# Performance work log

Hardware: AMD Instinct MI355X
Metric: run time of the kernel (lower is better)

Reference implementation:

```python
import jax, jax.numpy as jnp
import numpy as np

N_NODES = 100000
N_EDGES = 3200000
N_GRAPHS = 1024
IN_DIM, HID, OUT = 1, 32, 32
BN_EPS = 1e-5


def setup_inputs() -> dict:
    key = jax.random.key(0)
    ks = jax.random.split(key, 12)
    inp = {
        "x": jax.random.normal(ks[0], (N_NODES, IN_DIM), dtype=jnp.float32),
        "edge_index": jax.random.randint(ks[1], (2, N_EDGES), 0, N_NODES, dtype=jnp.int64),
        "batch": jnp.sort(jax.random.randint(ks[2], (N_NODES,), 0, N_GRAPHS, dtype=jnp.int64)),
        # GCNConv linear weights (out = x @ W + b) and BatchNorm (eval-mode) params
        "W1": jax.random.normal(ks[3], (IN_DIM, HID), dtype=jnp.float32) / np.sqrt(IN_DIM),
        "b1": jnp.zeros((HID,), jnp.float32),
        "bn1_g": jnp.ones((HID,), jnp.float32),
        "bn1_b": jnp.zeros((HID,), jnp.float32),
        "bn1_m": jax.random.normal(ks[4], (HID,), dtype=jnp.float32) * 0.1,
        "bn1_v": jnp.ones((HID,), jnp.float32),
        "W2": jax.random.normal(ks[5], (HID, HID), dtype=jnp.float32) / np.sqrt(HID),
        "b2": jnp.zeros((HID,), jnp.float32),
        "bn2_g": jnp.ones((HID,), jnp.float32),
        "bn2_b": jnp.zeros((HID,), jnp.float32),
        "bn2_m": jax.random.normal(ks[6], (HID,), dtype=jnp.float32) * 0.1,
        "bn2_v": jnp.ones((HID,), jnp.float32),
        "W3": jax.random.normal(ks[7], (HID, OUT), dtype=jnp.float32) / np.sqrt(HID),
        "b3": jnp.zeros((OUT,), jnp.float32),
    }
    return inp


def _gcn_norm(edge_index, n_nodes):
    # add self loops, compute sym-normalized edge weights (PyG GCNConv default)
    loop = jnp.arange(n_nodes, dtype=edge_index.dtype)
    src = jnp.concatenate([edge_index[0], loop])
    dst = jnp.concatenate([edge_index[1], loop])
    deg = jax.ops.segment_sum(jnp.ones_like(dst, dtype=jnp.float32), dst, num_segments=n_nodes)
    dinv = jnp.where(deg > 0, jax.lax.rsqrt(deg), 0.0)
    norm = dinv[src] * dinv[dst]  # [E + N]
    return src, dst, norm


def _gcn_conv(x, src, dst, norm, W, b, n_nodes):
    h = x @ W                                   # [N, F_out]
    msg = h[src] * norm[:, None]                # gather + scale, [E+N, F_out]
    out = jax.ops.segment_sum(msg, dst, num_segments=n_nodes)  # scatter-add
    return out + b


def _bn_eval(x, g, b, m, v):
    return (x - m) * jax.lax.rsqrt(v + BN_EPS) * g + b


def reference(x, edge_index, batch, W1, b1, bn1_g, bn1_b, bn1_m, bn1_v,
              W2, b2, bn2_g, bn2_b, bn2_m, bn2_v, W3, b3):
    n = x.shape[0]
    src, dst, norm = _gcn_norm(edge_index, n)
    h = _gcn_conv(x, src, dst, norm, W1, b1, n)
    h = jax.nn.relu(_bn_eval(h, bn1_g, bn1_b, bn1_m, bn1_v))  # dropout = id (eval)
    h = _gcn_conv(h, src, dst, norm, W2, b2, n)
    h = jax.nn.relu(_bn_eval(h, bn2_g, bn2_b, bn2_m, bn2_v))
    h = _gcn_conv(h, src, dst, norm, W3, b3, n)
    # global mean pool over graphs
    sums = jax.ops.segment_sum(h, batch, num_segments=N_GRAPHS)
    cnts = jax.ops.segment_sum(jnp.ones((n,), h.dtype), batch, num_segments=N_GRAPHS)
    return sums / jnp.maximum(cnts, 1.0)[:, None]
```

## Files before the change

kernel.cpp:

```cpp
#include <hip/hip_runtime.h>

#define N_NODES 100000
#define N_EDGES 3200000
#define N_GRAPHS 1024
#define HID 32
#define BN_EPS 1e-5f
#define NB 256

#define NBKT 512
#define NPB 196
#define PART_TILE 4096
#define PART_THREADS 256
#define PART_EPT (PART_TILE / PART_THREADS)


__device__ __forceinline__ int lbound(const int* __restrict__ a, int n, int key) {
    int lo = 0, hi = n;
    while (lo < hi) {
        int mid = (lo + hi) >> 1;
        if (a[mid] < key) lo = mid + 1; else hi = mid;
    }
    return lo;
}

__device__ __forceinline__ float bf2f(unsigned short h) {
    return __uint_as_float((unsigned)h << 16);
}
__device__ __forceinline__ unsigned short f2bf(float x) {
    unsigned u = __float_as_uint(x);
    u += 0x7fffu + ((u >> 16) & 1u);
    return (unsigned short)(u >> 16);
}


__global__ void k_zero(int* __restrict__ bhist) {
    bhist[threadIdx.x] = 0;
}

__global__ void k_hist(const int* __restrict__ dst, int* __restrict__ bhist) {
    __shared__ int h[NBKT];
    for (int i = threadIdx.x; i < NBKT; i += NB) h[i] = 0;
    __syncthreads();
    for (int e = blockIdx.x * NB + threadIdx.x; e < N_EDGES; e += gridDim.x * NB)
        atomicAdd(&h[dst[e] / NPB], 1);
    __syncthreads();
    for (int i = threadIdx.x; i < NBKT; i += NB)
        if (h[i]) atomicAdd(&bhist[i], h[i]);
}

__global__ void k_scan512(const int* __restrict__ bhist, int* __restrict__ bstart,
                          int* __restrict__ bcursor) {
    __shared__ int sm[NBKT];
    int t = threadIdx.x;
    int orig = bhist[t];
    sm[t] = orig;
    __syncthreads();
    for (int off = 1; off < NBKT; off <<= 1) {
        int v = (t >= off) ? sm[t - off] : 0;
        __syncthreads();
        sm[t] += v;
        __syncthreads();
    }
    int ex = sm[t] - orig;
    bstart[t] = ex;
    bcursor[t] = ex;
    if (t == NBKT - 1) bstart[NBKT] = sm[t];
}

__global__ void k_partition(const int* __restrict__ src, const int* __restrict__ dst,
                            int* __restrict__ bcursor,
                            unsigned long long* __restrict__ ebuf) {
    __shared__ int lh[NBKT];
    __shared__ int lcur[NBKT];
    const int tile0 = blockIdx.x * PART_TILE;
    for (int i = threadIdx.x; i < NBKT; i += PART_THREADS) lh[i] = 0;
    __syncthreads();
    int s[PART_EPT], d[PART_EPT], bk[PART_EPT];
#pragma unroll
    for (int k = 0; k < PART_EPT; ++k) {
        int e = tile0 + k * PART_THREADS + threadIdx.x;
        bool ok = (e < N_EDGES);
        s[k] = ok ? src[e] : 0;
        d[k] = ok ? dst[e] : 0;
        bk[k] = ok ? (d[k] / NPB) : -1;
        if (ok) atomicAdd(&lh[bk[k]], 1);
    }
    __syncthreads();
    for (int i = threadIdx.x; i < NBKT; i += PART_THREADS)
        lcur[i] = lh[i] ? atomicAdd(&bcursor[i], lh[i]) : 0;
    __syncthreads();
#pragma unroll
    for (int k = 0; k < PART_EPT; ++k) {
        if (bk[k] >= 0) {
            int pos = atomicAdd(&lcur[bk[k]], 1);
            ebuf[pos] = ((unsigned long long)(unsigned)d[k] << 32) | (unsigned)s[k];
        }
    }
}

__global__ void k_bucket(const int* __restrict__ bstart,
                         const unsigned long long* __restrict__ ebuf,
                         const float* __restrict__ x,
                         int* __restrict__ rowstart, int* __restrict__ deg,
                         float* __restrict__ dinv, float* __restrict__ zs1,
                         int* __restrict__ csr) {
    __shared__ int hist[NPB];
    __shared__ int sm[256];
    __shared__ int lcur[NPB];
    const int b = blockIdx.x;
    const int node0 = b * NPB;
    const int nn = N_NODES - node0;
    const int elo = bstart[b], ehi = bstart[b + 1];
    const int t = threadIdx.x;

    for (int i = t; i < NPB; i += blockDim.x) hist[i] = 0;
    __syncthreads();
    for (int e = elo + t; e < ehi; e += blockDim.x) {
        int dv = (int)(ebuf[e] >> 32);
        atomicAdd(&hist[dv - node0], 1);
    }
    __syncthreads();
    int orig = 0;
    if (t < 256) { orig = (t < NPB) ? hist[t] : 0; sm[t] = orig; }
    __syncthreads();
    for (int off = 1; off < 256; off <<= 1) {
        int v = 0;
        if (t < 256 && t >= off) v = sm[t - off];
        __syncthreads();
        if (t < 256) sm[t] += v;
        __syncthreads();
    }
    if (t < NPB) {
        int ex = sm[t] - orig;
        lcur[t] = ex;
        if (t < nn) {
            int node = node0 + t;
            rowstart[node] = elo + ex;
            deg[node] = orig;
            float di = rsqrtf((float)(orig + 1));
            dinv[node] = di;
            zs1[node] = di * x[node];
        }
    }
    __syncthreads();
    for (int e = elo + t; e < ehi; e += blockDim.x) {
        unsigned long long pk = ebuf[e];
        int dv = (int)(pk >> 32) - node0;
        int pos = atomicAdd(&lcur[dv], 1);
        csr[elo + pos] = (int)(pk & 0xffffffffu);
    }
}


__global__ void k_gather1(const int* __restrict__ rowstart, const int* __restrict__ deg,
                          const int* __restrict__ csr, const float* __restrict__ dinv,
                          const float* __restrict__ zs1, float* __restrict__ s) {
    int v = blockIdx.x * NB + threadIdx.x;
    if (v < N_NODES) {
        int lo = rowstart[v], n = deg[v];
        float acc = zs1[v];
        int j = 0;
        for (; j + 4 <= n; j += 4) {
            int u0 = csr[lo + j], u1 = csr[lo + j + 1];
            int u2 = csr[lo + j + 2], u3 = csr[lo + j + 3];
            float a0 = zs1[u0], a1 = zs1[u1], a2 = zs1[u2], a3 = zs1[u3];
            acc += (a0 + a1) + (a2 + a3);
        }
        for (; j < n; ++j) acc += zs1[csr[lo + j]];
        s[v] = dinv[v] * acc;
    }
}

__global__ void k_l1post(const float* __restrict__ s, const float* __restrict__ W1,
                         const float* __restrict__ b1, const float* __restrict__ g,
                         const float* __restrict__ bb, const float* __restrict__ m,
                         const float* __restrict__ v, const float* __restrict__ dinv,
                         unsigned short* __restrict__ zs2h) {
    int t = blockIdx.x * NB + threadIdx.x;
    if (t < N_NODES * HID) {
        int i = t >> 5, f = t & 31;
        float h = s[i] * W1[f] + b1[f];
        float scale = g[f] * rsqrtf(v[f] + BN_EPS);
        float z = fmaxf((h - m[f]) * scale + bb[f], 0.0f);
        zs2h[t] = f2bf(dinv[i] * z);
    }
}


__global__ void k_gather2(const int* __restrict__ rowstart, const int* __restrict__ deg,
                          const int* __restrict__ csr, const float* __restrict__ dinv,
                          const unsigned short* __restrict__ zs2h,
                          const float* __restrict__ W2,
                          const float* __restrict__ b2, const float* __restrict__ g2,
                          const float* __restrict__ bb2, const float* __restrict__ m2,
                          const float* __restrict__ v2, unsigned short* __restrict__ zs3h) {
    __shared__ float Ws[HID * HID];
    __shared__ float rowbuf[NB / HID][HID + 1];
    for (int k = threadIdx.x; k < HID * HID; k += NB) Ws[k] = W2[k];

    int t = blockIdx.x * NB + threadIdx.x;
    int v = t >> 5, f = t & 31, r = threadIdx.x >> 5;
    float acc = 0.0f, di = 0.0f;
    if (v < N_NODES) {
        di = dinv[v];
        int lo = rowstart[v], n = deg[v];
        acc = bf2f(zs2h[v * HID + f]);
        int j = 0;
        for (; j + 4 <= n; j += 4) {
            int u0 = csr[lo + j], u1 = csr[lo + j + 1];
            int u2 = csr[lo + j + 2], u3 = csr[lo + j + 3];
            float a0 = bf2f(zs2h[u0 * HID + f]);
            float a1 = bf2f(zs2h[u1 * HID + f]);
            float a2 = bf2f(zs2h[u2 * HID + f]);
            float a3 = bf2f(zs2h[u3 * HID + f]);
            acc += (a0 + a1) + (a2 + a3);
        }
        for (; j < n; ++j) acc += bf2f(zs2h[csr[lo + j] * HID + f]);
        acc *= di;
    }
    rowbuf[r][f] = acc;
    __syncthreads();
    if (v < N_NODES) {
        float h = b2[f];
#pragma unroll
        for (int k = 0; k < HID; ++k) h += rowbuf[r][k] * Ws[k * HID + f];
        float scale = g2[f] * rsqrtf(v2[f] + BN_EPS);
        float z = fmaxf((h - m2[f]) * scale + bb2[f], 0.0f);
        zs3h[v * HID + f] = f2bf(di * z);
    }
}


__global__ void k_gather3(const int* __restrict__ rowstart, const int* __restrict__ deg,
                          const int* __restrict__ csr, const float* __restrict__ dinv,
                          const unsigned short* __restrict__ zs3h,
                          float* __restrict__ agg3) {
    int t = blockIdx.x * NB + threadIdx.x;
    int v = t >> 5, f = t & 31;
    if (v < N_NODES) {
        int lo = rowstart[v], n = deg[v];
        float acc = bf2f(zs3h[v * HID + f]);
        int j = 0;
        for (; j + 4 <= n; j += 4) {
            int u0 = csr[lo + j], u1 = csr[lo + j + 1];
            int u2 = csr[lo + j + 2], u3 = csr[lo + j + 3];
            float a0 = bf2f(zs3h[u0 * HID + f]);
            float a1 = bf2f(zs3h[u1 * HID + f]);
            float a2 = bf2f(zs3h[u2 * HID + f]);
            float a3 = bf2f(zs3h[u3 * HID + f]);
            acc += (a0 + a1) + (a2 + a3);
        }
        for (; j < n; ++j) acc += bf2f(zs3h[csr[lo + j] * HID + f]);
        agg3[v * HID + f] = dinv[v] * acc;
    }
}


__global__ void k_pool(const float* __restrict__ agg3, const int* __restrict__ batch,
                       const float* __restrict__ W3, const float* __restrict__ b3,
                       float* __restrict__ out) {
    __shared__ float Ws[HID * HID];
    __shared__ float part[NB / HID][HID + 1];
    __shared__ float mrow[HID];
    int g = blockIdx.x;
    for (int k = threadIdx.x; k < HID * HID; k += NB) Ws[k] = W3[k];

    int lo = lbound(batch, N_NODES, g);
    int hi = lbound(batch, N_NODES, g + 1);

    int r = threadIdx.x >> 5, f = threadIdx.x & 31;
    float acc = 0.0f;
    for (int i = lo + r; i < hi; i += NB / HID) acc += agg3[i * HID + f];
    part[r][f] = acc;
    __syncthreads();
    if (threadIdx.x < HID) {
        float srow = 0.0f;
#pragma unroll
        for (int k = 0; k < NB / HID; ++k) srow += part[k][threadIdx.x];
        float c = (float)(hi - lo);
        mrow[threadIdx.x] = (hi > lo) ? srow / c : 0.0f;
    }
    __syncthreads();
    if (threadIdx.x < HID) {
        int ff = threadIdx.x;
        float o = 0.0f;
        if (hi > lo) {
            o = b3[ff];
#pragma unroll
            for (int k = 0; k < HID; ++k) o += mrow[k] * Ws[k * HID + ff];
        }
        out[g * HID + ff] = o;
    }
}


extern "C" void kernel_launch(void* const* d_in, const int* in_sizes, int n_in,
                              void* d_out, int out_size, void* d_ws, size_t ws_size,
                              hipStream_t stream) {
    const float* x     = (const float*)d_in[0];
    const int*   eidx  = (const int*)d_in[1];
    const int*   batch = (const int*)d_in[2];
    const float* W1    = (const float*)d_in[3];
    const float* b1    = (const float*)d_in[4];
    const float* bn1g  = (const float*)d_in[5];
    const float* bn1b  = (const float*)d_in[6];
    const float* bn1m  = (const float*)d_in[7];
    const float* bn1v  = (const float*)d_in[8];
    const float* W2    = (const float*)d_in[9];
    const float* b2    = (const float*)d_in[10];
    const float* bn2g  = (const float*)d_in[11];
    const float* bn2b  = (const float*)d_in[12];
    const float* bn2m  = (const float*)d_in[13];
    const float* bn2v  = (const float*)d_in[14];
    const float* W3    = (const float*)d_in[15];
    const float* b3    = (const float*)d_in[16];
    float* out = (float*)d_out;

    const int* src = eidx;
    const int* dst = eidx + N_EDGES;

    char* ws = (char*)d_ws;
    size_t off = 0;
    auto carve = [&](size_t bytes) {
        void* p = ws + off;
        off += (bytes + 255) & ~size_t(255);
        return p;
    };
    int*   bhist    = (int*)carve(NBKT * 4);
    int*   bstart   = (int*)carve((NBKT + 1) * 4);
    int*   bcursor  = (int*)carve(NBKT * 4);
    int*   rowstart = (int*)carve(N_NODES * 4);
    int*   deg      = (int*)carve(N_NODES * 4);
    float* dinv     = (float*)carve(N_NODES * 4);
    float* zs1      = (float*)carve(N_NODES * 4);
    float* s        = (float*)carve(N_NODES * 4);
    int*   csr      = (int*)carve((size_t)N_EDGES * 4);
    char*  region   = (char*)carve((size_t)N_EDGES * 8);
    unsigned long long* ebuf = (unsigned long long*)region;
    unsigned short* zs2h = (unsigned short*)region;
    unsigned short* zs3h = (unsigned short*)(region + (size_t)N_NODES * HID * 2);
    float* agg3          = (float*)(region + (size_t)N_NODES * HID * 4);

    const int gN   = (N_NODES + NB - 1) / NB;
    const int gNF  = (N_NODES * HID + NB - 1) / NB;
    const int gPart = (N_EDGES + PART_TILE - 1) / PART_TILE;

    k_zero<<<1, NBKT, 0, stream>>>(bhist);
    k_hist<<<1024, NB, 0, stream>>>(dst, bhist);
    k_scan512<<<1, NBKT, 0, stream>>>(bhist, bstart, bcursor);
    k_partition<<<gPart, PART_THREADS, 0, stream>>>(src, dst, bcursor, ebuf);
    k_bucket<<<NBKT, 512, 0, stream>>>(bstart, ebuf, x, rowstart, deg, dinv, zs1, csr);
    k_gather1<<<gN, NB, 0, stream>>>(rowstart, deg, csr, dinv, zs1, s);
    k_l1post<<<gNF, NB, 0, stream>>>(s, W1, b1, bn1g, bn1b, bn1m, bn1v, dinv, zs2h);
    k_gather2<<<gNF, NB, 0, stream>>>(rowstart, deg, csr, dinv, zs2h,
                                      W2, b2, bn2g, bn2b, bn2m, bn2v, zs3h);
    k_gather3<<<gNF, NB, 0, stream>>>(rowstart, deg, csr, dinv, zs3h, agg3);
    k_pool<<<N_GRAPHS, NB, 0, stream>>>(agg3, batch, W3, b3, out);
}
```

Before: 282.4 us.

## Fuse layer-1 post into gather2, pack edges to 32-bit, bf16 agg3, nontemporal loads

Removes the k_l1post kernel. gather2 now recomputes each neighbour's layer-1 activation on the fly from a packed (s*dinv, dinv) float2, so it never materialises or reads the bf16 N×32 zs2 buffer. The partition buffer shrinks from 64-bit to 32-bit entries (local dst offset in the high bits, src in the low 17 bits). The layer-3 aggregate is stored as bf16, the gather loops unroll to 8, and streaming index reads use nontemporal loads. These cut memory traffic and one launch, at the cost of extra per-edge ALU work in gather2 and lower precision in the pooled aggregate.

```diff
diff --git a/kernel.cpp b/kernel.cpp
--- a/kernel.cpp
+++ b/kernel.cpp
@@ -42,7 +42,7 @@
     for (int i = threadIdx.x; i < NBKT; i += NB) h[i] = 0;
     __syncthreads();
     for (int e = blockIdx.x * NB + threadIdx.x; e < N_EDGES; e += gridDim.x * NB)
-        atomicAdd(&h[dst[e] / NPB], 1);
+        atomicAdd(&h[__builtin_nontemporal_load(&dst[e]) / NPB], 1);
     __syncthreads();
     for (int i = threadIdx.x; i < NBKT; i += NB)
         if (h[i]) atomicAdd(&bhist[i], h[i]);
@@ -68,21 +68,22 @@
 }
 
 __global__ void k_partition(const int* __restrict__ src, const int* __restrict__ dst,
-                            int* __restrict__ bcursor,
-                            unsigned long long* __restrict__ ebuf) {
+                            int* __restrict__ bcursor, unsigned* __restrict__ ebuf) {
     __shared__ int lh[NBKT];
     __shared__ int lcur[NBKT];
     const int tile0 = blockIdx.x * PART_TILE;
     for (int i = threadIdx.x; i < NBKT; i += PART_THREADS) lh[i] = 0;
     __syncthreads();
-    int s[PART_EPT], d[PART_EPT], bk[PART_EPT];
+    int s[PART_EPT], bk[PART_EPT], dl[PART_EPT];
 #pragma unroll
     for (int k = 0; k < PART_EPT; ++k) {
         int e = tile0 + k * PART_THREADS + threadIdx.x;
         bool ok = (e < N_EDGES);
-        s[k] = ok ? src[e] : 0;
-        d[k] = ok ? dst[e] : 0;
-        bk[k] = ok ? (d[k] / NPB) : -1;
+        int sv = ok ? __builtin_nontemporal_load(&src[e]) : 0;
+        int dv = ok ? __builtin_nontemporal_load(&dst[e]) : 0;
+        s[k] = sv;
+        bk[k] = ok ? (dv / NPB) : -1;
+        dl[k] = dv - bk[k] * NPB;
         if (ok) atomicAdd(&lh[bk[k]], 1);
     }
     __syncthreads();
@@ -93,13 +94,13 @@
     for (int k = 0; k < PART_EPT; ++k) {
         if (bk[k] >= 0) {
             int pos = atomicAdd(&lcur[bk[k]], 1);
-            ebuf[pos] = ((unsigned long long)(unsigned)d[k] << 32) | (unsigned)s[k];
+            ebuf[pos] = ((unsigned)dl[k] << 17) | (unsigned)s[k];
         }
     }
 }
 
 __global__ void k_bucket(const int* __restrict__ bstart,
-                         const unsigned long long* __restrict__ ebuf,
+                         const unsigned* __restrict__ ebuf,
                          const float* __restrict__ x,
                          int* __restrict__ rowstart, int* __restrict__ deg,
                          float* __restrict__ dinv, float* __restrict__ zs1,
@@ -115,10 +116,8 @@
 
     for (int i = t; i < NPB; i += blockDim.x) hist[i] = 0;
     __syncthreads();
-    for (int e = elo + t; e < ehi; e += blockDim.x) {
-        int dv = (int)(ebuf[e] >> 32);
-        atomicAdd(&hist[dv - node0], 1);
-    }
+    for (int e = elo + t; e < ehi; e += blockDim.x)
+        atomicAdd(&hist[ebuf[e] >> 17], 1);
     __syncthreads();
     int orig = 0;
     if (t < 256) { orig = (t < NPB) ? hist[t] : 0; sm[t] = orig; }
@@ -144,52 +143,40 @@
     }
     __syncthreads();
     for (int e = elo + t; e < ehi; e += blockDim.x) {
-        unsigned long long pk = ebuf[e];
-        int dv = (int)(pk >> 32) - node0;
-        int pos = atomicAdd(&lcur[dv], 1);
-        csr[elo + pos] = (int)(pk & 0xffffffffu);
+        unsigned pk = ebuf[e];
+        int pos = atomicAdd(&lcur[pk >> 17], 1);
+        csr[elo + pos] = (int)(pk & 0x1FFFFu);
     }
 }
 
 
 __global__ void k_gather1(const int* __restrict__ rowstart, const int* __restrict__ deg,
                           const int* __restrict__ csr, const float* __restrict__ dinv,
-                          const float* __restrict__ zs1, float* __restrict__ s) {
+                          const float* __restrict__ zs1, float2* __restrict__ sd) {
     int v = blockIdx.x * NB + threadIdx.x;
     if (v < N_NODES) {
         int lo = rowstart[v], n = deg[v];
         float acc = zs1[v];
         int j = 0;
         for (; j + 4 <= n; j += 4) {
-            int u0 = csr[lo + j], u1 = csr[lo + j + 1];
-            int u2 = csr[lo + j + 2], u3 = csr[lo + j + 3];
+            int u0 = __builtin_nontemporal_load(&csr[lo + j]);
+            int u1 = __builtin_nontemporal_load(&csr[lo + j + 1]);
+            int u2 = __builtin_nontemporal_load(&csr[lo + j + 2]);
+            int u3 = __builtin_nontemporal_load(&csr[lo + j + 3]);
             float a0 = zs1[u0], a1 = zs1[u1], a2 = zs1[u2], a3 = zs1[u3];
             acc += (a0 + a1) + (a2 + a3);
         }
         for (; j < n; ++j) acc += zs1[csr[lo + j]];
-        s[v] = dinv[v] * acc;
-    }
-}
-
-__global__ void k_l1post(const float* __restrict__ s, const float* __restrict__ W1,
-                         const float* __restrict__ b1, const float* __restrict__ g,
-                         const float* __restrict__ bb, const float* __restrict__ m,
-                         const float* __restrict__ v, const float* __restrict__ dinv,
-                         unsigned short* __restrict__ zs2h) {
-    int t = blockIdx.x * NB + threadIdx.x;
-    if (t < N_NODES * HID) {
-        int i = t >> 5, f = t & 31;
-        float h = s[i] * W1[f] + b1[f];
-        float scale = g[f] * rsqrtf(v[f] + BN_EPS);
-        float z = fmaxf((h - m[f]) * scale + bb[f], 0.0f);
-        zs2h[t] = f2bf(dinv[i] * z);
-    }
-}
-
+        float di = dinv[v];
+        sd[v] = make_float2(di * acc, di);
+    }
+}
 
 __global__ void k_gather2(const int* __restrict__ rowstart, const int* __restrict__ deg,
-                          const int* __restrict__ csr, const float* __restrict__ dinv,
-                          const unsigned short* __restrict__ zs2h,
+                          const int* __restrict__ csr, const float2* __restrict__ sd,
+                          const float* __restrict__ W1, const float* __restrict__ b1,
+                          const float* __restrict__ g1, const float* __restrict__ bb1,
+                          const float* __restrict__ m1, const float* __restrict__ v1,
                           const float* __restrict__ W2,
                           const float* __restrict__ b2, const float* __restrict__ g2,
                           const float* __restrict__ bb2, const float* __restrict__ m2,
@@ -200,22 +187,41 @@
 
     int t = blockIdx.x * NB + threadIdx.x;
     int v = t >> 5, f = t & 31, r = threadIdx.x >> 5;
+    float sc1 = g1[f] * rsqrtf(v1[f] + BN_EPS);
+    float A = W1[f] * sc1;
+    float Bc = (b1[f] - m1[f]) * sc1 + bb1[f];
     float acc = 0.0f, di = 0.0f;
     if (v < N_NODES) {
-        di = dinv[v];
+        float2 pv = sd[v];
+        di = pv.y;
+        acc = di * fmaxf(pv.x * A + Bc, 0.0f);
         int lo = rowstart[v], n = deg[v];
-        acc = bf2f(zs2h[v * HID + f]);
         int j = 0;
-        for (; j + 4 <= n; j += 4) {
-            int u0 = csr[lo + j], u1 = csr[lo + j + 1];
-            int u2 = csr[lo + j + 2], u3 = csr[lo + j + 3];
-            float a0 = bf2f(zs2h[u0 * HID + f]);
-            float a1 = bf2f(zs2h[u1 * HID + f]);
-            float a2 = bf2f(zs2h[u2 * HID + f]);
-            float a3 = bf2f(zs2h[u3 * HID + f]);
-            acc += (a0 + a1) + (a2 + a3);
-        }
-        for (; j < n; ++j) acc += bf2f(zs2h[csr[lo + j] * HID + f]);
+        for (; j + 8 <= n; j += 8) {
+            int u0 = __builtin_nontemporal_load(&csr[lo + j]);
+            int u1 = __builtin_nontemporal_load(&csr[lo + j + 1]);
+            int u2 = __builtin_nontemporal_load(&csr[lo + j + 2]);
+            int u3 = __builtin_nontemporal_load(&csr[lo + j + 3]);
+            int u4 = __builtin_nontemporal_load(&csr[lo + j + 4]);
+            int u5 = __builtin_nontemporal_load(&csr[lo + j + 5]);
+            int u6 = __builtin_nontemporal_load(&csr[lo + j + 6]);
+            int u7 = __builtin_nontemporal_load(&csr[lo + j + 7]);
+            float2 p0 = sd[u0], p1 = sd[u1], p2 = sd[u2], p3 = sd[u3];
+            float2 p4 = sd[u4], p5 = sd[u5], p6 = sd[u6], p7 = sd[u7];
+            float a0 = p0.y * fmaxf(p0.x * A + Bc, 0.0f);
+            float a1 = p1.y * fmaxf(p1.x * A + Bc, 0.0f);
+            float a2 = p2.y * fmaxf(p2.x * A + Bc, 0.0f);
+            float a3 = p3.y * fmaxf(p3.x * A + Bc, 0.0f);
+            float a4 = p4.y * fmaxf(p4.x * A + Bc, 0.0f);
+            float a5 = p5.y * fmaxf(p5.x * A + Bc, 0.0f);
+            float a6 = p6.y * fmaxf(p6.x * A + Bc, 0.0f);
+            float a7 = p7.y * fmaxf(p7.x * A + Bc, 0.0f);
+            acc += ((a0 + a1) + (a2 + a3)) + ((a4 + a5) + (a6 + a7));
+        }
+        for (; j < n; ++j) {
+            float2 p = sd[csr[lo + j]];
+            acc += p.y * fmaxf(p.x * A + Bc, 0.0f);
+        }
         acc *= di;
     }
     rowbuf[r][f] = acc;
@@ -224,8 +230,8 @@
         float h = b2[f];
 #pragma unroll
         for (int k = 0; k < HID; ++k) h += rowbuf[r][k] * Ws[k * HID + f];
-        float scale = g2[f] * rsqrtf(v2[f] + BN_EPS);
-        float z = fmaxf((h - m2[f]) * scale + bb2[f], 0.0f);
+        float sc2 = g2[f] * rsqrtf(v2[f] + BN_EPS);
+        float z = fmaxf((h - m2[f]) * sc2 + bb2[f], 0.0f);
         zs3h[v * HID + f] = f2bf(di * z);
     }
 }
@@ -234,29 +240,40 @@
 __global__ void k_gather3(const int* __restrict__ rowstart, const int* __restrict__ deg,
                           const int* __restrict__ csr, const float* __restrict__ dinv,
                           const unsigned short* __restrict__ zs3h,
-                          float* __restrict__ agg3) {
+                          unsigned short* __restrict__ agg3h) {
     int t = blockIdx.x * NB + threadIdx.x;
     int v = t >> 5, f = t & 31;
     if (v < N_NODES) {
         int lo = rowstart[v], n = deg[v];
         float acc = bf2f(zs3h[v * HID + f]);
         int j = 0;
-        for (; j + 4 <= n; j += 4) {
-            int u0 = csr[lo + j], u1 = csr[lo + j + 1];
-            int u2 = csr[lo + j + 2], u3 = csr[lo + j + 3];
+        for (; j + 8 <= n; j += 8) {
+            int u0 = __builtin_nontemporal_load(&csr[lo + j]);
+            int u1 = __builtin_nontemporal_load(&csr[lo + j + 1]);
+            int u2 = __builtin_nontemporal_load(&csr[lo + j + 2]);
+            int u3 = __builtin_nontemporal_load(&csr[lo + j + 3]);
+            int u4 = __builtin_nontemporal_load(&csr[lo + j + 4]);
+            int u5 = __builtin_nontemporal_load(&csr[lo + j + 5]);
+            int u6 = __builtin_nontemporal_load(&csr[lo + j + 6]);
+            int u7 = __builtin_nontemporal_load(&csr[lo + j + 7]);
             float a0 = bf2f(zs3h[u0 * HID + f]);
             float a1 = bf2f(zs3h[u1 * HID + f]);
             float a2 = bf2f(zs3h[u2 * HID + f]);
             float a3 = bf2f(zs3h[u3 * HID + f]);
-            acc += (a0 + a1) + (a2 + a3);
+            float a4 = bf2f(zs3h[u4 * HID + f]);
+            float a5 = bf2f(zs3h[u5 * HID + f]);
+            float a6 = bf2f(zs3h[u6 * HID + f]);
+            float a7 = bf2f(zs3h[u7 * HID + f]);
+            acc += ((a0 + a1) + (a2 + a3)) + ((a4 + a5) + (a6 + a7));
         }
         for (; j < n; ++j) acc += bf2f(zs3h[csr[lo + j] * HID + f]);
-        agg3[v * HID + f] = dinv[v] * acc;
-    }
-}
-
-
-__global__ void k_pool(const float* __restrict__ agg3, const int* __restrict__ batch,
+        __builtin_nontemporal_store(f2bf(dinv[v] * acc), &agg3h[v * HID + f]);
+    }
+}
+
+
+__global__ void k_pool(const unsigned short* __restrict__ agg3h,
+                       const int* __restrict__ batch,
                        const float* __restrict__ W3, const float* __restrict__ b3,
                        float* __restrict__ out) {
     __shared__ float Ws[HID * HID];
@@ -270,7 +287,8 @@
 
     int r = threadIdx.x >> 5, f = threadIdx.x & 31;
     float acc = 0.0f;
-    for (int i = lo + r; i < hi; i += NB / HID) acc += agg3[i * HID + f];
+    for (int i = lo + r; i < hi; i += NB / HID)
+        acc += bf2f(__builtin_nontemporal_load(&agg3h[i * HID + f]));
     part[r][f] = acc;
     __syncthreads();
     if (threadIdx.x < HID) {
@@ -326,23 +344,22 @@
         off += (bytes + 255) & ~size_t(255);
         return p;
     };
-    int*   bhist    = (int*)carve(NBKT * 4);
-    int*   bstart   = (int*)carve((NBKT + 1) * 4);
-    int*   bcursor  = (int*)carve(NBKT * 4);
-    int*   rowstart = (int*)carve(N_NODES * 4);
-    int*   deg      = (int*)carve(N_NODES * 4);
-    float* dinv     = (float*)carve(N_NODES * 4);
-    float* zs1      = (float*)carve(N_NODES * 4);
-    float* s        = (float*)carve(N_NODES * 4);
-    int*   csr      = (int*)carve((size_t)N_EDGES * 4);
-    char*  region   = (char*)carve((size_t)N_EDGES * 8);
-    unsigned long long* ebuf = (unsigned long long*)region;
-    unsigned short* zs2h = (unsigned short*)region;
-    unsigned short* zs3h = (unsigned short*)(region + (size_t)N_NODES * HID * 2);
-    float* agg3          = (float*)(region + (size_t)N_NODES * HID * 4);
-
-    const int gN   = (N_NODES + NB - 1) / NB;
-    const int gNF  = (N_NODES * HID + NB - 1) / NB;
+    int*    bhist    = (int*)carve(NBKT * 4);
+    int*    bstart   = (int*)carve((NBKT + 1) * 4);
+    int*    bcursor  = (int*)carve(NBKT * 4);
+    int*    rowstart = (int*)carve(N_NODES * 4);
+    int*    deg      = (int*)carve(N_NODES * 4);
+    float*  dinv     = (float*)carve(N_NODES * 4);
+    float*  zs1      = (float*)carve(N_NODES * 4);
+    float2* sd       = (float2*)carve((size_t)N_NODES * 8);
+    int*    csr      = (int*)carve((size_t)N_EDGES * 4);
+    char*   region   = (char*)carve((size_t)N_EDGES * 4);
+    unsigned*       ebuf  = (unsigned*)region;
+    unsigned short* zs3h  = (unsigned short*)region;
+    unsigned short* agg3h = (unsigned short*)(region + (size_t)N_NODES * HID * 2);
+
+    const int gN    = (N_NODES + NB - 1) / NB;
+    const int gNF   = (N_NODES * HID + NB - 1) / NB;
     const int gPart = (N_EDGES + PART_TILE - 1) / PART_TILE;
 
     k_zero<<<1, NBKT, 0, stream>>>(bhist);
@@ -350,10 +367,10 @@
     k_scan512<<<1, NBKT, 0, stream>>>(bhist, bstart, bcursor);
     k_partition<<<gPart, PART_THREADS, 0, stream>>>(src, dst, bcursor, ebuf);
     k_bucket<<<NBKT, 512, 0, stream>>>(bstart, ebuf, x, rowstart, deg, dinv, zs1, csr);
-    k_gather1<<<gN, NB, 0, stream>>>(rowstart, deg, csr, dinv, zs1, s);
-    k_l1post<<<gNF, NB, 0, stream>>>(s, W1, b1, bn1g, bn1b, bn1m, bn1v, dinv, zs2h);
-    k_gather2<<<gNF, NB, 0, stream>>>(rowstart, deg, csr, dinv, zs2h,
+    k_gather1<<<gN, NB, 0, stream>>>(rowstart, deg, csr, dinv, zs1, sd);
+    k_gather2<<<gNF, NB, 0, stream>>>(rowstart, deg, csr, sd,
+                                      W1, b1, bn1g, bn1b, bn1m, bn1v,
                                       W2, b2, bn2g, bn2b, bn2m, bn2v, zs3h);
-    k_gather3<<<gNF, NB, 0, stream>>>(rowstart, deg, csr, dinv, zs3h, agg3);
-    k_pool<<<N_GRAPHS, NB, 0, stream>>>(agg3, batch, W3, b3, out);
-}
+    k_gather3<<<gNF, NB, 0, stream>>>(rowstart, deg, csr, dinv, zs3h, agg3h);
+    k_pool<<<N_GRAPHS, NB, 0, stream>>>(agg3h, batch, W3, b3, out);
+}
```

Result: slower. 296.2 us (+4.9%).
